# Kernel tuning notes

Measured on AMD Instinct MI355X. Metric: run time of the kernel, lower is better.

## Reference

```python
import jax, jax.numpy as jnp
import numpy as np

D_MODEL = 1024
N_HEADS = 16
D_HEAD = D_MODEL // N_HEADS
IGNORE = -100000.0


def setup_inputs() -> dict:
    key = jax.random.key(0)
    ks = jax.random.split(key, 12)
    B, S = 4, 2048
    x_q = jax.random.normal(ks[0], (B, S, D_MODEL), dtype=jnp.float32)
    x_kv = jax.random.normal(ks[1], (B, S, D_MODEL), dtype=jnp.float32)
    # mask[q, k] == True means the score is replaced with IGNORE (masked out)
    mask = jax.random.randint(ks[2], (S, S), 0, 2) == 1
    sq = 1.0 / np.sqrt(D_MODEL)
    sh = 1.0 / np.sqrt(D_HEAD)
    W_Q = jax.random.normal(ks[3], (N_HEADS, D_MODEL, D_HEAD), dtype=jnp.float32) * sq
    W_K = jax.random.normal(ks[4], (N_HEADS, D_MODEL, D_HEAD), dtype=jnp.float32) * sq
    W_V = jax.random.normal(ks[5], (N_HEADS, D_MODEL, D_HEAD), dtype=jnp.float32) * sq
    W_O = jax.random.normal(ks[6], (N_HEADS, D_HEAD, D_MODEL), dtype=jnp.float32) * sh
    b_Q = jnp.zeros((N_HEADS, D_HEAD), dtype=jnp.float32)
    b_K = jnp.zeros((N_HEADS, D_HEAD), dtype=jnp.float32)
    b_V = jnp.zeros((N_HEADS, D_HEAD), dtype=jnp.float32)
    b_O = jnp.zeros((D_MODEL,), dtype=jnp.float32)
    return {"x_q": x_q, "x_kv": x_kv, "mask": mask,
            "W_Q": W_Q, "W_K": W_K, "W_V": W_V, "W_O": W_O,
            "b_Q": b_Q, "b_K": b_K, "b_V": b_V, "b_O": b_O}


def reference(x_q, x_kv, mask, W_Q, W_K, W_V, W_O, b_Q, b_K, b_V, b_O):
    # per-head QKV projections: b s d, n d h -> b s n h
    q = jnp.einsum('bsd,ndh->bsnh', x_q, W_Q) + b_Q
    k = jnp.einsum('bsd,ndh->bsnh', x_kv, W_K) + b_K
    v = jnp.einsum('bsd,ndh->bsnh', x_kv, W_V) + b_V
    scale = 1.0 / np.sqrt(D_HEAD)  # flex_attention default scaling
    # scores: [B, H, Sq, Sk]
    scores = jnp.einsum('bqnh,bknh->bnqk', q, k) * scale
    # score_mod: where mask True -> IGNORE
    scores = jnp.where(mask[None, None, :, :], jnp.float32(IGNORE), scores)
    attn = jax.nn.softmax(scores, axis=-1)
    z = jnp.einsum('bnqk,bknh->bqnh', attn, v)  # [B, Sq, H, Dh]
    # per-head output projection then sum over heads
    out = jnp.einsum('bqnh,nhd->bqd', z, W_O) + b_O
    return (out, z)
```

## Files before the change

kernel.cpp:

```cpp
#include <hip/hip_runtime.h>

#define S_LEN 2048
#define NHEAD 16
#define DHEAD 64
#define DMODEL 1024
#define BATCH 4
#define SC2 0.18033688011112042f

typedef short bf16x8 __attribute__((ext_vector_type(8)));
typedef float f32x4 __attribute__((ext_vector_type(4)));
typedef unsigned short u16;
typedef unsigned short u16x8 __attribute__((ext_vector_type(8)));
typedef unsigned short u16x4 __attribute__((ext_vector_type(4)));
typedef unsigned long long u64;
typedef unsigned long long u64x2 __attribute__((ext_vector_type(2)));

__device__ __forceinline__ u16 f2b(float f) {
  unsigned u = __builtin_bit_cast(unsigned, f);
  u += 0x7FFFu + ((u >> 16) & 1u);
  return (u16)(u >> 16);
}
__device__ __forceinline__ float b2f(u16 v) {
  unsigned u = ((unsigned)v) << 16;
  return __builtin_bit_cast(float, u);
}
__device__ __forceinline__ f32x4 mfma16(bf16x8 a, bf16x8 b, f32x4 c) {
  return __builtin_amdgcn_mfma_f32_16x16x32_bf16(a, b, c, 0, 0, 0);
}
__device__ __forceinline__ void load_lds16(const void* g, void* l) {
  __builtin_amdgcn_global_load_lds(
      (const __attribute__((address_space(1))) unsigned int*)g,
      (__attribute__((address_space(3))) unsigned int*)l, 16, 0, 0);
}
__device__ __forceinline__ float fexp2(float x) {
  float r;
  asm("v_exp_f32 %0, %1\n\ts_nop 1" : "=v"(r) : "v"(x));
  return r;
}
__device__ __forceinline__ unsigned cvtpk(float lo, float hi) {
  unsigned r;
  asm("v_cvt_pk_bf16_f32 %0, %1, %2" : "=v"(r) : "v"(lo), "v"(hi));
  return r;
}


__global__ void cvt_f32_bf16(const float* __restrict__ src, u16* __restrict__ dst, int n4) {
  int i = blockIdx.x * 256 + threadIdx.x;
  int stride = gridDim.x * 256;
  for (; i < n4; i += stride) {
    float4 v = ((const float4*)src)[i];
    u16x4 o = { f2b(v.x), f2b(v.y), f2b(v.z), f2b(v.w) };
    ((u16x4*)dst)[i] = o;
  }
}

__global__ void mask_expand(const int* __restrict__ M, u64* __restrict__ Mex) {
  int idx = blockIdx.x * 256 + threadIdx.x;
  int q = idx >> 9, k = (idx & 511) * 4;
  int4 v = *(const int4*)(M + (size_t)q * S_LEN + k);
  int T = k >> 6, t = (k >> 4) & 3, g = (k >> 2) & 3;
  u64 m = 0;
  if (!v.x) m |= 0xFFFFull;
  if (!v.y) m |= 0xFFFF0000ull;
  if (!v.z) m |= 0xFFFF00000000ull;
  if (!v.w) m |= 0xFFFF000000000000ull;
  Mex[((size_t)q * 32 + T) * 16 + g * 4 + t] = m;
}

__global__ void repack_w(const float* __restrict__ W, u16* __restrict__ WT, float scale) {
  __shared__ u16 t[64][66];
  const int tid = threadIdx.x;
  const int n = blockIdx.y, d0 = blockIdx.x * 64;
  const float* src = W + (size_t)n * 65536;
  for (int p = 0; p < 4; ++p) {
    int idx = p * 256 + tid;
    int r = idx >> 4, cs = idx & 15;
    float4 v = *(const float4*)(src + (size_t)(d0 + r) * 64 + cs * 4);
    t[r][cs*4+0] = f2b(v.x*scale); t[r][cs*4+1] = f2b(v.y*scale);
    t[r][cs*4+2] = f2b(v.z*scale); t[r][cs*4+3] = f2b(v.w*scale);
  }
  __syncthreads();
  for (int p = 0; p < 2; ++p) {
    int idx = p * 256 + tid;
    int hl = idx >> 3, ds = idx & 7;
    u16x8 o;
    for (int e = 0; e < 8; ++e) o[e] = t[ds*8+e][hl];
    *(u16x8*)(WT + (size_t)(n*64 + hl) * 1024 + d0 + ds*8) = o;
  }
}

__global__ void split_wo(const float* __restrict__ Wo, u16* __restrict__ Hi, u16* __restrict__ Lo) {
  __shared__ u16 th[64][66];
  __shared__ u16 tl[64][66];
  const int tid = threadIdx.x;
  const int d0 = blockIdx.x * 64, c0 = blockIdx.y * 64;
  for (int p = 0; p < 4; ++p) {
    int idx = p * 256 + tid;
    int r = idx >> 4, cs = idx & 15;
    float4 v = *(const float4*)(Wo + (size_t)(c0 + r) * 1024 + d0 + cs * 4);
    float f[4] = {v.x, v.y, v.z, v.w};
    for (int e = 0; e < 4; ++e) {
      u16 hb = f2b(f[e]);
      th[r][cs*4+e] = hb;
      tl[r][cs*4+e] = f2b(f[e] - b2f(hb));
    }
  }
  __syncthreads();
  for (int p = 0; p < 2; ++p) {
    int idx = p * 256 + tid;
    int dr = idx >> 3, cs = idx & 7;
    u16x8 oh, ol;
    for (int e = 0; e < 8; ++e) { oh[e] = th[cs*8+e][dr]; ol[e] = tl[cs*8+e][dr]; }
    *(u16x8*)(Hi + (size_t)(d0 + dr) * 1024 + c0 + cs*8) = oh;
    *(u16x8*)(Lo + (size_t)(d0 + dr) * 1024 + c0 + cs*8) = ol;
  }
}

__global__ void transpose_v(const u16* __restrict__ V, u16* __restrict__ VT) {
  __shared__ u16 t[64][66];
  const int tid = threadIdx.x;
  const int s0 = blockIdx.x * 64;
  const int b = blockIdx.y >> 4, h = blockIdx.y & 15;
  for (int p = 0; p < 2; ++p) {
    int idx = p * 256 + tid;
    int r = idx >> 3, sg = idx & 7;
    u16x8 v = *(const u16x8*)(V + (size_t)(b*S_LEN + s0 + r) * 1024 + h*64 + sg*8);
    for (int e = 0; e < 8; ++e) t[r][sg*8+e] = v[e];
  }
  __syncthreads();
  for (int p = 0; p < 2; ++p) {
    int idx = p * 256 + tid;
    int dr = idx >> 3, ss = idx & 7;
    u16x8 o;
    for (int e = 0; e < 8; ++e) o[e] = t[ss*8+e][dr];
    *(u16x8*)(VT + ((size_t)(b*NHEAD + h) * 64 + dr) * 2048 + s0 + ss*8) = o;
  }
}


template<int BF16OUT>
__global__ __launch_bounds__(256, 2)
void gemm_bt(const u16* __restrict__ A, const u16* __restrict__ Bt,
             const float* __restrict__ bias, float bscale, void* __restrict__ Cout)
{
  __shared__ __align__(16) char As[16384];
  __shared__ __align__(16) char Bs[16384];
  const int tid = threadIdx.x, wid = tid >> 6, lane = tid & 63;
  const int lq = lane & 15, g = lane >> 4;
  const size_t am0 = (size_t)blockIdx.y * 128;
  const size_t bn0 = (size_t)blockIdx.x * 128;
  const int wr = (wid >> 1) * 64, wc = (wid & 1) * 64;
  f32x4 z4 = {0.f, 0.f, 0.f, 0.f};
  f32x4 acc[4][4];
  for (int i = 0; i < 4; ++i) for (int j = 0; j < 4; ++j) acc[i][j] = z4;
  for (int k0 = 0; k0 < DMODEL; k0 += 64) {
#pragma unroll
    for (int c = 0; c < 4; ++c) {
      int idx = c*256 + tid, r = idx >> 3, s = idx & 7;
      load_lds16(A + (am0 + r)*DMODEL + k0 + ((s ^ (r & 7)) << 3), As + idx*16);
    }
#pragma unroll
    for (int c = 0; c < 4; ++c) {
      int idx = c*256 + tid, r = idx >> 3, s = idx & 7;
      load_lds16(Bt + (bn0 + r)*DMODEL + k0 + ((s ^ (r & 7)) << 3), Bs + idx*16);
    }
    __syncthreads();
#pragma unroll
    for (int ks = 0; ks < 2; ++ks) {
      bf16x8 af[4], bfr[4];
#pragma unroll
      for (int i = 0; i < 4; ++i) {
        int row = wr + i*16 + lq;
        af[i] = *(const bf16x8*)(As + row*128 + (((ks*4 + g) ^ (row & 7)) << 4));
      }
#pragma unroll
      for (int j = 0; j < 4; ++j) {
        int row = wc + j*16 + lq;
        bfr[j] = *(const bf16x8*)(Bs + row*128 + (((ks*4 + g) ^ (row & 7)) << 4));
      }
#pragma unroll
      for (int i = 0; i < 4; ++i)
#pragma unroll
        for (int j = 0; j < 4; ++j)
          acc[i][j] = mfma16(af[i], bfr[j], acc[i][j]);
    }
    __syncthreads();
  }
#pragma unroll
  for (int i = 0; i < 4; ++i)
#pragma unroll
    for (int j = 0; j < 4; ++j) {
      size_t row = am0 + wr + i*16 + g*4;
      int col = (int)bn0 + wc + j*16 + lq;
      float bv = bias[col] * bscale;
#pragma unroll
      for (int r = 0; r < 4; ++r) {
        float v = acc[i][j][r] + bv;
        if (BF16OUT) ((u16*)Cout)[(row + r)*DMODEL + col] = f2b(v);
        else         ((float*)Cout)[(row + r)*DMODEL + col] = v;
      }
    }
}


__global__ __launch_bounds__(256, 2)
void gemm_out(const float* __restrict__ Z, const u16* __restrict__ Bh,
              const u16* __restrict__ Bl, const float* __restrict__ bias,
              float* __restrict__ Cout)
{
  __shared__ __align__(16) char Ah[16384];
  __shared__ __align__(16) char Al[16384];
  __shared__ __align__(16) char Bhs[16384];
  __shared__ __align__(16) char Bls[16384];
  const int tid = threadIdx.x, wid = tid >> 6, lane = tid & 63;
  const int lq = lane & 15, g = lane >> 4;
  const size_t am0 = (size_t)blockIdx.y * 128;
  const size_t bn0 = (size_t)blockIdx.x * 128;
  const int wr = (wid >> 1) * 64, wc = (wid & 1) * 64;
  f32x4 z4 = {0.f, 0.f, 0.f, 0.f};
  f32x4 acc[4][4];
  for (int i = 0; i < 4; ++i) for (int j = 0; j < 4; ++j) acc[i][j] = z4;
  for (int k0 = 0; k0 < DMODEL; k0 += 64) {
#pragma unroll
    for (int c = 0; c < 8; ++c) {
      int idx = c*256 + tid, r = idx >> 4, fs = idx & 15;
      float4 v = *(const float4*)(Z + (am0 + r)*DMODEL + k0 + fs*4);
      float f[4] = {v.x, v.y, v.z, v.w};
      u16x4 hv, lv;
      for (int e = 0; e < 4; ++e) {
        u16 hb = f2b(f[e]);
        hv[e] = hb;
        lv[e] = f2b(f[e] - b2f(hb));
      }
      int byo = r*128 + ((((fs >> 1) ^ (r & 7)) << 4) | ((fs & 1) << 3));
      *(u16x4*)(Ah + byo) = hv;
      *(u16x4*)(Al + byo) = lv;
    }
#pragma unroll
    for (int c = 0; c < 4; ++c) {
      int idx = c*256 + tid, r = idx >> 3, s = idx & 7;
      load_lds16(Bh + (bn0 + r)*DMODEL + k0 + ((s ^ (r & 7)) << 3), Bhs + idx*16);
    }
#pragma unroll
    for (int c = 0; c < 4; ++c) {
      int idx = c*256 + tid, r = idx >> 3, s = idx & 7;
      load_lds16(Bl + (bn0 + r)*DMODEL + k0 + ((s ^ (r & 7)) << 3), Bls + idx*16);
    }
    __syncthreads();
#pragma unroll
    for (int ks = 0; ks < 2; ++ks) {
      bf16x8 ah[4], al[4], bh4[4], bl4[4];
#pragma unroll
      for (int i = 0; i < 4; ++i) {
        int row = wr + i*16 + lq;
        int off = row*128 + (((ks*4 + g) ^ (row & 7)) << 4);
        ah[i] = *(const bf16x8*)(Ah + off);
        al[i] = *(const bf16x8*)(Al + off);
      }
#pragma unroll
      for (int j = 0; j < 4; ++j) {
        int row = wc + j*16 + lq;
        int off = row*128 + (((ks*4 + g) ^ (row & 7)) << 4);
        bh4[j] = *(const bf16x8*)(Bhs + off);
        bl4[j] = *(const bf16x8*)(Bls + off);
      }
#pragma unroll
      for (int i = 0; i < 4; ++i)
#pragma unroll
        for (int j = 0; j < 4; ++j) {
          acc[i][j] = mfma16(al[i], bh4[j], acc[i][j]);
          acc[i][j] = mfma16(ah[i], bl4[j], acc[i][j]);
          acc[i][j] = mfma16(ah[i], bh4[j], acc[i][j]);
        }
    }
    __syncthreads();
  }
#pragma unroll
  for (int i = 0; i < 4; ++i)
#pragma unroll
    for (int j = 0; j < 4; ++j) {
      size_t row = am0 + wr + i*16 + g*4;
      int col = (int)bn0 + wc + j*16 + lq;
      float bv = bias[col];
#pragma unroll
      for (int r = 0; r < 4; ++r)
        Cout[(row + r)*DMODEL + col] = acc[i][j][r] + bv;
    }
}

__global__ __launch_bounds__(256, 3)
void attn(const u16* __restrict__ Q, const u16* __restrict__ K,
          const u16* __restrict__ VT, const u64* __restrict__ Mex,
          float* __restrict__ Zf)
{
  __shared__ __align__(16) char L[49152];
  const int tid = threadIdx.x, wid = tid >> 6, lane = tid & 63;
  const int lq = lane & 15, g = lane >> 4;
  const int Lb = blockIdx.x;
  const int xcd = Lb & 7, slot = Lb >> 3;
  const int qt = slot & 15, pl = slot >> 4;
  const int pair = xcd * 8 + pl;
  const int h = pair & 15, b = pair >> 4;
  const int q0 = qt * 128;
  const int qw = q0 + wid * 32;

  bf16x8 qf[2][2];
#pragma unroll
  for (int u = 0; u < 2; ++u) {
    const u16* qp = Q + (size_t)(b*S_LEN + qw + u*16 + lq) * DMODEL + h*DHEAD + g*8;
    qf[u][0] = *(const bf16x8*)qp;
    qf[u][1] = *(const bf16x8*)(qp + 32);
  }
  bf16x8 ones;
#pragma unroll
  for (int e = 0; e < 8; ++e) ones[e] = (short)0x3F80;

  const f32x4 z4 = {0.f, 0.f, 0.f, 0.f};
  f32x4 Oc[2][4];
#pragma unroll
  for (int u = 0; u < 2; ++u)
#pragma unroll
    for (int t = 0; t < 4; ++t) Oc[u][t] = z4;
  f32x4 lrow[2] = {z4, z4};

  const u16* kp = K + (size_t)(b*S_LEN)*DMODEL + h*DHEAD;
  const u16* vp = VT + (size_t)((b*NHEAD + h)*DHEAD)*S_LEN;
  const u64* mx0 = Mex + (size_t)(qw + lq) * 512 + g*4;
  const u64* mx1 = Mex + (size_t)(qw + 16 + lq) * 512 + g*4;
  char* myP = L + 32768 + wid*4096;

  size_t ko[2], vo[2];
  int sd[2];
#pragma unroll
  for (int c = 0; c < 2; ++c) {
    int idx = c*256 + tid, r = idx >> 3, s = idx & 7, so = (s ^ (r & 7)) << 3;
    ko[c] = (size_t)r * DMODEL + so;
    vo[c] = (size_t)r * S_LEN + so;
    sd[c] = idx * 16;
  }

  bf16x8 kr0, kr1, vr0, vr1;
  kr0 = *(const bf16x8*)(kp + ko[0]); kr1 = *(const bf16x8*)(kp + ko[1]);
  vr0 = *(const bf16x8*)(vp + vo[0]); vr1 = *(const bf16x8*)(vp + vo[1]);
  u64x2 m0a = *(const u64x2*)(mx0), m0b = *(const u64x2*)(mx0 + 2);
  u64x2 m1a = *(const u64x2*)(mx1), m1b = *(const u64x2*)(mx1 + 2);
  kp += 64*DMODEL; vp += 64;
  *(bf16x8*)(L + sd[0]) = kr0;  *(bf16x8*)(L + sd[1]) = kr1;
  *(bf16x8*)(L + 8192 + sd[0]) = vr0;  *(bf16x8*)(L + 8192 + sd[1]) = vr1;
  __syncthreads();

  for (int it = 0; it < 32; ++it) {
    char* Bu = L + (it & 1) * 16384;
    char* Bn = L + ((it + 1) & 1) * 16384;
    u64x2 n0a = {0,0}, n0b = {0,0}, n1a = {0,0}, n1b = {0,0};
    if (it < 31) {
      kr0 = *(const bf16x8*)(kp + ko[0]); kr1 = *(const bf16x8*)(kp + ko[1]);
      vr0 = *(const bf16x8*)(vp + vo[0]); vr1 = *(const bf16x8*)(vp + vo[1]);
      n0a = *(const u64x2*)(mx0 + (it+1)*16);
      n0b = *(const u64x2*)(mx0 + (it+1)*16 + 2);
      n1a = *(const u64x2*)(mx1 + (it+1)*16);
      n1b = *(const u64x2*)(mx1 + (it+1)*16 + 2);
      kp += 64*DMODEL; vp += 64;
    }

    f32x4 st[2][4];
    __builtin_amdgcn_s_setprio(1);
#pragma unroll
    for (int t = 0; t < 4; ++t) {
      int row = t*16 + lq;
      bf16x8 kf0 = *(const bf16x8*)(Bu + row*128 + ((g ^ (row & 7)) << 4));
      bf16x8 kf1 = *(const bf16x8*)(Bu + row*128 + (((4 + g) ^ (row & 7)) << 4));
      st[0][t] = mfma16(kf1, qf[0][1], mfma16(kf0, qf[0][0], z4));
      st[1][t] = mfma16(kf1, qf[1][1], mfma16(kf0, qf[1][0], z4));
    }
    __builtin_amdgcn_s_setprio(0);

#pragma unroll
    for (int u = 0; u < 2; ++u) {
      char* pb = myP + (u*16 + lq) * 128;
#pragma unroll
      for (int t = 0; t < 4; ++t) {
        int sl = (((t*2 + (g >> 1)) ^ (lq & 7)) << 4) + ((g & 1) << 3);
        float p0 = fexp2(st[u][t][0]);
        float p1 = fexp2(st[u][t][1]);
        float p2 = fexp2(st[u][t][2]);
        float p3 = fexp2(st[u][t][3]);
        u64 mt = u ? ((t < 2) ? m1a[t & 1] : m1b[t & 1])
                   : ((t < 2) ? m0a[t & 1] : m0b[t & 1]);
        union { unsigned w32[2]; u64 w64; } pw;
        pw.w32[0] = cvtpk(p0, p1);
        pw.w32[1] = cvtpk(p2, p3);
        *(u64*)(pb + sl) = pw.w64 & mt;
      }
    }
    asm volatile("s_waitcnt lgkmcnt(0)" ::: "memory");
    __builtin_amdgcn_sched_barrier(0);

    bf16x8 pf[2][2];
#pragma unroll
    for (int u = 0; u < 2; ++u) {
      char* pb = myP + (u*16 + lq) * 128;
      pf[u][0] = *(const bf16x8*)(pb + (((0 + g) ^ (lq & 7)) << 4));
      pf[u][1] = *(const bf16x8*)(pb + (((4 + g) ^ (lq & 7)) << 4));
    }

    __builtin_amdgcn_s_setprio(1);
    f32x4 ts0 = mfma16(pf[0][1], ones, mfma16(pf[0][0], ones, z4));
    f32x4 ts1 = mfma16(pf[1][1], ones, mfma16(pf[1][0], ones, z4));
#pragma unroll
    for (int t = 0; t < 4; ++t) {
      int row = t*16 + lq;
#pragma unroll
      for (int hh = 0; hh < 2; ++hh) {
        bf16x8 vf = *(const bf16x8*)(Bu + 8192 + row*128 + (((hh*4 + g) ^ (row & 7)) << 4));
        Oc[0][t] = mfma16(pf[0][hh], vf, Oc[0][t]);
        Oc[1][t] = mfma16(pf[1][hh], vf, Oc[1][t]);
      }
    }
    __builtin_amdgcn_s_setprio(0);
    lrow[0] += ts0;
    lrow[1] += ts1;

    if (it < 31) {
      *(bf16x8*)(Bn + sd[0]) = kr0;  *(bf16x8*)(Bn + sd[1]) = kr1;
      *(bf16x8*)(Bn + 8192 + sd[0]) = vr0;  *(bf16x8*)(Bn + 8192 + sd[1]) = vr1;
    }
    __syncthreads();
    m0a = n0a; m0b = n0b; m1a = n1a; m1b = n1b;
  }

#pragma unroll
  for (int u = 0; u < 2; ++u) {
    float i0 = 1.f / lrow[u][0], i1 = 1.f / lrow[u][1],
          i2 = 1.f / lrow[u][2], i3 = 1.f / lrow[u][3];
#pragma unroll
    for (int t = 0; t < 4; ++t) {
      size_t base = ((size_t)(b*S_LEN + qw + u*16 + g*4) * NHEAD + h) * DHEAD + t*16 + lq;
      Zf[base       ] = Oc[u][t][0] * i0;
      Zf[base + 1024] = Oc[u][t][1] * i1;
      Zf[base + 2048] = Oc[u][t][2] * i2;
      Zf[base + 3072] = Oc[u][t][3] * i3;
    }
  }
}


extern "C" void kernel_launch(void* const* d_in, const int* in_sizes, int n_in,
                              void* d_out, int out_size, void* d_ws, size_t ws_size,
                              hipStream_t stream) {
  const float* x_q  = (const float*)d_in[0];
  const float* x_kv = (const float*)d_in[1];
  const int*   mask = (const int*)d_in[2];
  const float* W_Q  = (const float*)d_in[3];
  const float* W_K  = (const float*)d_in[4];
  const float* W_V  = (const float*)d_in[5];
  const float* W_O  = (const float*)d_in[6];
  const float* b_Q  = (const float*)d_in[7];
  const float* b_K  = (const float*)d_in[8];
  const float* b_V  = (const float*)d_in[9];
  const float* b_O  = (const float*)d_in[10];

  if (ws_size < 102760448) return;

  u16* ws  = (u16*)d_ws;
  u16* XQ  = ws;
  u16* XKV = XQ  + 8388608;
  u16* WQT = XKV + 8388608;
  u16* WKT = WQT + 1048576;
  u16* WVT = WKT + 1048576;
  u16* WOH = WVT + 1048576;
  u16* WOL = WOH + 1048576;
  u16* Qb  = WOL + 1048576;
  u16* Kb  = Qb  + 8388608;
  u16* Vb  = Kb  + 8388608;
  u64* Mxp = (u64*)(Vb + 8388608);
  u16* VTp = XQ;

  float* out = (float*)d_out;
  float* zf  = out + 8388608;

  cvt_f32_bf16<<<2048, 256, 0, stream>>>(x_q,  XQ,  2097152);
  cvt_f32_bf16<<<2048, 256, 0, stream>>>(x_kv, XKV, 2097152);
  repack_w<<<dim3(16,16), 256, 0, stream>>>(W_Q, WQT, SC2);
  repack_w<<<dim3(16,16), 256, 0, stream>>>(W_K, WKT, 1.0f);
  repack_w<<<dim3(16,16), 256, 0, stream>>>(W_V, WVT, 1.0f);
  split_wo<<<dim3(16,16), 256, 0, stream>>>(W_O, WOH, WOL);
  mask_expand<<<4096, 256, 0, stream>>>(mask, Mxp);
  gemm_bt<1><<<dim3(8,64), 256, 0, stream>>>(XQ,  WQT, b_Q, SC2, Qb);
  gemm_bt<1><<<dim3(8,64), 256, 0, stream>>>(XKV, WKT, b_K, 1.0f, Kb);
  gemm_bt<1><<<dim3(8,64), 256, 0, stream>>>(XKV, WVT, b_V, 1.0f, Vb);
  transpose_v<<<dim3(32,64), 256, 0, stream>>>(Vb, VTp);
  attn<<<1024, 256, 0, stream>>>(Qb, Kb, VTp, Mxp, zf);
  gemm_out<<<dim3(8,64), 256, 0, stream>>>(zf, WOH, WOL, b_O, out);
}
```

Baseline: 283.1 us.

## Single-buffer K/V LDS in attention to fit four blocks per CU

Replaces the double-buffered K/V shared-memory tiles with one buffer, shrinking LDS from 48KB to 32KB, and raises launch bounds from 3 to 4 blocks per CU. An extra barrier is added before the register-staged next tile is written, so compute and the LDS store no longer overlap inside a block. Global prefetch into registers is kept. The four exp instructions are also batched into one asm block sharing a single s_nop, cutting per-exp padding.

```diff
diff --git a/kernel.cpp b/kernel.cpp
--- a/kernel.cpp
+++ b/kernel.cpp
@@ -32,10 +32,13 @@
       (const __attribute__((address_space(1))) unsigned int*)g,
       (__attribute__((address_space(3))) unsigned int*)l, 16, 0, 0);
 }
-__device__ __forceinline__ float fexp2(float x) {
-  float r;
-  asm("v_exp_f32 %0, %1\n\ts_nop 1" : "=v"(r) : "v"(x));
-  return r;
+__device__ __forceinline__ void fexp2x4(float& a, float& b, float& c, float& d) {
+  asm("v_exp_f32 %0, %0\n\t"
+      "v_exp_f32 %1, %1\n\t"
+      "v_exp_f32 %2, %2\n\t"
+      "v_exp_f32 %3, %3\n\t"
+      "s_nop 1"
+      : "+v"(a), "+v"(b), "+v"(c), "+v"(d));
 }
 __device__ __forceinline__ unsigned cvtpk(float lo, float hi) {
   unsigned r;
@@ -288,12 +291,12 @@
     }
 }
 
-__global__ __launch_bounds__(256, 3)
+__global__ __launch_bounds__(256, 4)
 void attn(const u16* __restrict__ Q, const u16* __restrict__ K,
           const u16* __restrict__ VT, const u64* __restrict__ Mex,
           float* __restrict__ Zf)
 {
-  __shared__ __align__(16) char L[49152];
+  __shared__ __align__(16) char L[32768];
   const int tid = threadIdx.x, wid = tid >> 6, lane = tid & 63;
   const int lq = lane & 15, g = lane >> 4;
   const int Lb = blockIdx.x;
@@ -327,7 +330,7 @@
   const u16* vp = VT + (size_t)((b*NHEAD + h)*DHEAD)*S_LEN;
   const u64* mx0 = Mex + (size_t)(qw + lq) * 512 + g*4;
   const u64* mx1 = Mex + (size_t)(qw + 16 + lq) * 512 + g*4;
-  char* myP = L + 32768 + wid*4096;
+  char* myP = L + 16384 + wid*4096;
 
   size_t ko[2], vo[2];
   int sd[2];
@@ -350,8 +353,6 @@
   __syncthreads();
 
   for (int it = 0; it < 32; ++it) {
-    char* Bu = L + (it & 1) * 16384;
-    char* Bn = L + ((it + 1) & 1) * 16384;
     u64x2 n0a = {0,0}, n0b = {0,0}, n1a = {0,0}, n1b = {0,0};
     if (it < 31) {
       kr0 = *(const bf16x8*)(kp + ko[0]); kr1 = *(const bf16x8*)(kp + ko[1]);
@@ -368,8 +369,8 @@
 #pragma unroll
     for (int t = 0; t < 4; ++t) {
       int row = t*16 + lq;
-      bf16x8 kf0 = *(const bf16x8*)(Bu + row*128 + ((g ^ (row & 7)) << 4));
-      bf16x8 kf1 = *(const bf16x8*)(Bu + row*128 + (((4 + g) ^ (row & 7)) << 4));
+      bf16x8 kf0 = *(const bf16x8*)(L + row*128 + ((g ^ (row & 7)) << 4));
+      bf16x8 kf1 = *(const bf16x8*)(L + row*128 + (((4 + g) ^ (row & 7)) << 4));
       st[0][t] = mfma16(kf1, qf[0][1], mfma16(kf0, qf[0][0], z4));
       st[1][t] = mfma16(kf1, qf[1][1], mfma16(kf0, qf[1][0], z4));
     }
@@ -381,10 +382,9 @@
 #pragma unroll
       for (int t = 0; t < 4; ++t) {
         int sl = (((t*2 + (g >> 1)) ^ (lq & 7)) << 4) + ((g & 1) << 3);
-        float p0 = fexp2(st[u][t][0]);
-        float p1 = fexp2(st[u][t][1]);
-        float p2 = fexp2(st[u][t][2]);
-        float p3 = fexp2(st[u][t][3]);
+        float p0 = st[u][t][0], p1 = st[u][t][1];
+        float p2 = st[u][t][2], p3 = st[u][t][3];
+        fexp2x4(p0, p1, p2, p3);
         u64 mt = u ? ((t < 2) ? m1a[t & 1] : m1b[t & 1])
                    : ((t < 2) ? m0a[t & 1] : m0b[t & 1]);
         union { unsigned w32[2]; u64 w64; } pw;
@@ -412,7 +412,7 @@
       int row = t*16 + lq;
 #pragma unroll
       for (int hh = 0; hh < 2; ++hh) {
-        bf16x8 vf = *(const bf16x8*)(Bu + 8192 + row*128 + (((hh*4 + g) ^ (row & 7)) << 4));
+        bf16x8 vf = *(const bf16x8*)(L + 8192 + row*128 + (((hh*4 + g) ^ (row & 7)) << 4));
         Oc[0][t] = mfma16(pf[0][hh], vf, Oc[0][t]);
         Oc[1][t] = mfma16(pf[1][hh], vf, Oc[1][t]);
       }
@@ -421,9 +421,10 @@
     lrow[0] += ts0;
     lrow[1] += ts1;
 
+    __syncthreads();
     if (it < 31) {
-      *(bf16x8*)(Bn + sd[0]) = kr0;  *(bf16x8*)(Bn + sd[1]) = kr1;
-      *(bf16x8*)(Bn + 8192 + sd[0]) = vr0;  *(bf16x8*)(Bn + 8192 + sd[1]) = vr1;
+      *(bf16x8*)(L + sd[0]) = kr0;  *(bf16x8*)(L + sd[1]) = kr1;
+      *(bf16x8*)(L + 8192 + sd[0]) = vr0;  *(bf16x8*)(L + 8192 + sd[1]) = vr1;
     }
     __syncthreads();
     m0a = n0a; m0b = n0b; m1a = n1a; m1b = n1b;
```

Measured after the change: 548.9 us. 93.9% more time.
